# Kernel tuning notes

Hardware: AMD Instinct MI355X
Metric: run time of the kernel (lower is better)

## Reference

```python
import jax, jax.numpy as jnp
import numpy as np

B, T, NF, D = 512, 24, 81, 64
NH, HD = 4, 16
EPS = 1e-5


def _ln(x, g, b):
    m = x.mean(-1, keepdims=True)
    v = ((x - m) ** 2).mean(-1, keepdims=True)
    return (x - m) * jax.lax.rsqrt(v + EPS) * g + b


def _glu(h, w1, b1, w2, b2):
    return jax.nn.sigmoid(h @ w1 + b1) * (h @ w2 + b2)


def setup_inputs() -> dict:
    key = jax.random.key(0)
    ki = iter(jax.random.split(key, 64))

    def w(*shape):
        return jax.random.normal(next(ki), shape, jnp.float32) * 0.05

    FD = NF * D
    inp = {
        "x": jax.random.normal(next(ki), (B, T, NF), jnp.float32),
        # 81 per-feature GRNs, stacked along axis 0 (feature axis)
        "f_w1": w(NF, D), "f_b1": w(NF, D),
        "f_w2": w(NF, D, D), "f_b2": w(NF, D),
        "f_g1w": w(NF, D, D), "f_g1b": w(NF, D),
        "f_g2w": w(NF, D, D), "f_g2b": w(NF, D),
        "f_skw": w(NF, D), "f_skb": w(NF, D),
        "f_lng": jnp.ones((NF, D), jnp.float32), "f_lnb": jnp.zeros((NF, D), jnp.float32),
        # weight GRN: 5184 -> 64 -> 81
        "w_w1": w(FD, D), "w_b1": w(D),
        "w_w2": w(D, NF), "w_b2": w(NF),
        "w_g1w": w(NF, NF), "w_g1b": w(NF),
        "w_g2w": w(NF, NF), "w_g2b": w(NF),
        "w_skw": w(FD, NF), "w_skb": w(NF),
        "w_lng": jnp.ones((NF,), jnp.float32), "w_lnb": jnp.zeros((NF,), jnp.float32),
        # LSTM (torch layout: [4H, in], gate order i,f,g,o)
        "lstm_wih": w(4 * D, D), "lstm_whh": w(4 * D, D),
        "lstm_bih": w(4 * D), "lstm_bhh": w(4 * D),
        # post-lstm GLU + LN
        "pl_g1w": w(D, D), "pl_g1b": w(D), "pl_g2w": w(D, D), "pl_g2b": w(D),
        "pl_lng": jnp.ones((D,), jnp.float32), "pl_lnb": jnp.zeros((D,), jnp.float32),
        # MHA (in-proj packed q,k,v; weights stored [in, out])
        "attn_in_w": w(D, 3 * D), "attn_in_b": w(3 * D),
        "attn_out_w": w(D, D), "attn_out_b": w(D),
        # post-attn GLU + LN
        "pa_g1w": w(D, D), "pa_g1b": w(D), "pa_g2w": w(D, D), "pa_g2b": w(D),
        "pa_lng": jnp.ones((D,), jnp.float32), "pa_lnb": jnp.zeros((D,), jnp.float32),
        # feed-forward GRN (skip = identity since d_in == d_out)
        "ff_w1": w(D, 2 * D), "ff_b1": w(2 * D),
        "ff_w2": w(2 * D, D), "ff_b2": w(D),
        "ff_g1w": w(D, D), "ff_g1b": w(D), "ff_g2w": w(D, D), "ff_g2b": w(D),
        "ff_lng": jnp.ones((D,), jnp.float32), "ff_lnb": jnp.zeros((D,), jnp.float32),
        # output head
        "fc1_w": w(D, D), "fc1_b": w(D),
        "fc2_w": w(D, 6), "fc2_b": w(6),
    }
    return inp


def _forward(x, f_w1, f_b1, f_w2, f_b2, f_g1w, f_g1b, f_g2w, f_g2b, f_skw, f_skb,
             f_lng, f_lnb,
             w_w1, w_b1, w_w2, w_b2, w_g1w, w_g1b, w_g2w, w_g2b, w_skw, w_skb,
             w_lng, w_lnb,
             lstm_wih, lstm_whh, lstm_bih, lstm_bhh,
             pl_g1w, pl_g1b, pl_g2w, pl_g2b, pl_lng, pl_lnb,
             attn_in_w, attn_in_b, attn_out_w, attn_out_b,
             pa_g1w, pa_g1b, pa_g2w, pa_g2b, pa_lng, pa_lnb,
             ff_w1, ff_b1, ff_w2, ff_b2, ff_g1w, ff_g1b, ff_g2w, ff_g2b,
             ff_lng, ff_lnb,
             fc1_w, fc1_b, fc2_w, fc2_b):
    Bv, Tv = x.shape[0], x.shape[1]
    # --- VSN: 81 per-feature GRNs, vectorized over the feature axis ---
    h = jax.nn.elu(x[..., None] * f_w1 + f_b1)                    # [B,T,F,D]
    h = jnp.einsum('btfi,fio->btfo', h, f_w2) + f_b2
    h = jax.nn.sigmoid(jnp.einsum('btfi,fio->btfo', h, f_g1w) + f_g1b) \
        * (jnp.einsum('btfi,fio->btfo', h, f_g2w) + f_g2b)
    res = x[..., None] * f_skw + f_skb                            # skip: Linear(1,D)
    stacked = _ln(h + res, f_lng, f_lnb)                          # [B,T,F,D]
    flat = stacked.reshape(Bv, Tv, NF * D)
    # weight GRN -> softmax over features
    wh = jax.nn.elu(flat @ w_w1 + w_b1)
    wh = wh @ w_w2 + w_b2
    wh = _glu(wh, w_g1w, w_g1b, w_g2w, w_g2b)
    wnorm = _ln(wh + flat @ w_skw + w_skb, w_lng, w_lnb)
    weights = jax.nn.softmax(wnorm, axis=-1)                      # [B,T,F]
    selected = jnp.einsum('btfd,btf->btd', stacked, weights)      # [B,T,D]

    # --- LSTM encoder (single layer) ---
    def step(carry, xt):
        hp, cp = carry
        gates = xt @ lstm_wih.T + hp @ lstm_whh.T + lstm_bih + lstm_bhh
        i, f, g, o = jnp.split(gates, 4, axis=-1)
        c = jax.nn.sigmoid(f) * cp + jax.nn.sigmoid(i) * jnp.tanh(g)
        hn = jax.nn.sigmoid(o) * jnp.tanh(c)
        return (hn, c), hn

    h0 = jnp.zeros((Bv, D), x.dtype)
    _, hs = jax.lax.scan(step, (h0, h0), selected.transpose(1, 0, 2))
    lstm_out = hs.transpose(1, 0, 2)                              # [B,T,D]

    temporal = _ln(_glu(lstm_out, pl_g1w, pl_g1b, pl_g2w, pl_g2b) + selected,
                   pl_lng, pl_lnb)

    # --- Multi-head self-attention ---
    qkv = temporal @ attn_in_w + attn_in_b                        # [B,T,3D]
    q, k, v = jnp.split(qkv, 3, axis=-1)

    def heads(t):
        return t.reshape(Bv, Tv, NH, HD).transpose(0, 2, 1, 3)

    q, k, v = heads(q), heads(k), heads(v)
    scores = jnp.einsum('bhqd,bhkd->bhqk', q, k) / jnp.sqrt(jnp.float32(HD))
    a = jax.nn.softmax(scores, axis=-1)
    ao = jnp.einsum('bhqk,bhkd->bhqd', a, v).transpose(0, 2, 1, 3).reshape(Bv, Tv, D)
    attn_out = ao @ attn_out_w + attn_out_b

    enriched = _ln(_glu(attn_out, pa_g1w, pa_g1b, pa_g2w, pa_g2b) + temporal,
                   pa_lng, pa_lnb)

    # --- FF GRN (identity skip) ---
    fh = jax.nn.elu(enriched @ ff_w1 + ff_b1)
    fh = fh @ ff_w2 + ff_b2
    fh = _glu(fh, ff_g1w, ff_g1b, ff_g2w, ff_g2b)
    out = _ln(fh + enriched, ff_lng, ff_lnb)

    pooled = out.mean(axis=1)                                     # [B,D]
    return jax.nn.relu(pooled @ fc1_w + fc1_b) @ fc2_w + fc2_b    # [B,6]


def reference(x, f_w1, f_b1, f_w2, f_b2, f_g1w, f_g1b, f_g2w, f_g2b, f_skw, f_skb,
              f_lng, f_lnb,
              w_w1, w_b1, w_w2, w_b2, w_g1w, w_g1b, w_g2w, w_g2b, w_skw, w_skb,
              w_lng, w_lnb,
              lstm_wih, lstm_whh, lstm_bih, lstm_bhh,
              pl_g1w, pl_g1b, pl_g2w, pl_g2b, pl_lng, pl_lnb,
              attn_in_w, attn_in_b, attn_out_w, attn_out_b,
              pa_g1w, pa_g1b, pa_g2w, pa_g2b, pa_lng, pa_lnb,
              ff_w1, ff_b1, ff_w2, ff_b2, ff_g1w, ff_g1b, ff_g2w, ff_g2b,
              ff_lng, ff_lnb,
              fc1_w, fc1_b, fc2_w, fc2_b):
    return _forward(x, f_w1, f_b1, f_w2, f_b2, f_g1w, f_g1b, f_g2w, f_g2b, f_skw,
                    f_skb, f_lng, f_lnb, w_w1, w_b1, w_w2, w_b2, w_g1w, w_g1b,
                    w_g2w, w_g2b, w_skw, w_skb, w_lng, w_lnb, lstm_wih, lstm_whh,
                    lstm_bih, lstm_bhh, pl_g1w, pl_g1b, pl_g2w, pl_g2b, pl_lng,
                    pl_lnb, attn_in_w, attn_in_b, attn_out_w, attn_out_b, pa_g1w,
                    pa_g1b, pa_g2w, pa_g2b, pa_lng, pa_lnb, ff_w1, ff_b1, ff_w2,
                    ff_b2, ff_g1w, ff_g1b, ff_g2w, ff_g2b, ff_lng, ff_lnb, fc1_w,
                    fc1_b, fc2_w, fc2_b)
```

## Files before the change

### kernel.cpp

```cpp
#include <hip/hip_runtime.h>
#include <hip/hip_bf16.h>
#include <math.h>

constexpr int BB   = 512;
constexpr int TSEQ = 24;
constexpr int NF   = 81;
constexpr int DD   = 64;
constexpr int MTOT = BB * TSEQ;
constexpr int FDIM = NF * DD;
constexpr int KS   = 6;
constexpr int KSL  = 864;
constexpr int NW   = 160;
constexpr int NT   = 6;
constexpr float LN_EPS = 1e-5f;

typedef __attribute__((ext_vector_type(8))) short short8v;
typedef __attribute__((ext_vector_type(4))) float f32x4;

static __device__ __forceinline__ float sigmoidf_(float x) {
    return __builtin_amdgcn_rcpf(1.f + __expf(-x));
}
static __device__ __forceinline__ float eluf_(float x) {
    return x > 0.f ? x : (__expf(x) - 1.f);
}
static __device__ __forceinline__ float ftanh_(float x) {
    float e = __expf(2.f * x);
    return 1.f - 2.f * __builtin_amdgcn_rcpf(e + 1.f);
}
static __device__ __forceinline__ unsigned short f2bf(float x) {
    __hip_bfloat16 h = __float2bfloat16(x);
    return *reinterpret_cast<unsigned short*>(&h);
}
static __device__ __forceinline__ float b2f(unsigned short u) {
    __hip_bfloat16 h = *reinterpret_cast<__hip_bfloat16*>(&u);
    return __bfloat162float(h);
}

__global__ __launch_bounds__(256) void xt_kernel(
    const float* __restrict__ x, float* __restrict__ xT)
{
    __shared__ float tile[128 * 81];
    const int m0 = blockIdx.x * 128;
    const int t  = threadIdx.x;
    for (int e = t; e < 128 * 81; e += 256)
        tile[e] = x[(size_t)m0 * NF + e];
    __syncthreads();
    for (int e = t; e < 128 * 81; e += 256) {
        int f = e >> 7, r = e & 127;
        xT[(size_t)f * MTOT + m0 + r] = tile[r * 81 + f];
    }
}

__global__ __launch_bounds__(256) void vsn_kernel(
    const float* __restrict__ xT,
    const float* __restrict__ f_w1,  const float* __restrict__ f_b1,
    const float* __restrict__ f_w2,  const float* __restrict__ f_b2,
    const float* __restrict__ f_g1w, const float* __restrict__ f_g1b,
    const float* __restrict__ f_g2w, const float* __restrict__ f_g2b,
    const float* __restrict__ f_skw, const float* __restrict__ f_skb,
    const float* __restrict__ f_lng, const float* __restrict__ f_lnb,
    __hip_bfloat16* __restrict__ stacked)
{
    const int f  = blockIdx.y;
    const int t  = threadIdx.x;
    const int w  = t >> 6;
    const int l  = t & 63;
    const int lr = l & 15;
    const int lg = l >> 4;

    __shared__ __align__(16) unsigned short W2t[64 * 72];
    __shared__ __align__(16) unsigned short G1t[64 * 72];
    __shared__ __align__(16) unsigned short G2t[64 * 72];
    __shared__ __align__(16) unsigned short hS[4][16 * 72];
    __shared__ float vw1[64], vb1[64], vb2[64], vg1b[64], vg2b[64];
    __shared__ float vskw[64], vskb[64], vlng[64], vlnb[64];

    if (t < 64) {
        vw1[t]  = f_w1 [f*64 + t];  vb1[t]  = f_b1 [f*64 + t];
        vb2[t]  = f_b2 [f*64 + t];
        vg1b[t] = f_g1b[f*64 + t];  vg2b[t] = f_g2b[f*64 + t];
        vskw[t] = f_skw[f*64 + t];  vskb[t] = f_skb[f*64 + t];
        vlng[t] = f_lng[f*64 + t];  vlnb[t] = f_lnb[f*64 + t];
    }
    {
        const float* w2p = f_w2  + (size_t)f * 4096;
        const float* g1p = f_g1w + (size_t)f * 4096;
        const float* g2p = f_g2w + (size_t)f * 4096;
        #pragma unroll
        for (int p = 0; p < 16; ++p) {
            int e = t + 256 * p; int k = e >> 6, c = e & 63;
            W2t[c*72 + k] = f2bf(w2p[k*64 + c]);
            G1t[c*72 + k] = f2bf(g1p[k*64 + c]);
            G2t[c*72 + k] = f2bf(g2p[k*64 + c]);
        }
    }
    __syncthreads();

    unsigned short* slab = hS[w];

    for (int it = 0; it < NT; ++it) {
        const int m0 = (blockIdx.x * NT + it) * 64;
        const float xval = xT[(size_t)f * MTOT + m0 + w*16 + lr];

        short8v a0f, a1f;
        #pragma unroll
        for (int j = 0; j < 8; ++j) {
            const int d0 = lg*8 + j, d1 = 32 + lg*8 + j;
            a0f[j] = (short)f2bf(eluf_(xval * vw1[d0] + vb1[d0]));
            a1f[j] = (short)f2bf(eluf_(xval * vw1[d1] + vb1[d1]));
        }

        f32x4 acc1[4];
        #pragma unroll
        for (int cf = 0; cf < 4; ++cf) acc1[cf] = (f32x4){0.f,0.f,0.f,0.f};
        #pragma unroll
        for (int cf = 0; cf < 4; ++cf) {
            short8v b0 = *(const short8v*)&W2t[(cf*16 + lr)*72 + lg*8];
// ... 109 lines not shown
        short8v a0 = *(const short8v*)(stacked + a0r + k);
        short8v a1 = *(const short8v*)(stacked + a1r + k);
        #pragma unroll
        for (int n = 0; n < 10; ++n) {
            short8v bf = *(const short8v*)(WcatT + (size_t)(n*16 + lr) * FDIM + k);
            acc[0][n] = __builtin_amdgcn_mfma_f32_16x16x32_bf16(a0, bf, acc[0][n], 0, 0, 0);
            acc[1][n] = __builtin_amdgcn_mfma_f32_16x16x32_bf16(a1, bf, acc[1][n], 0, 0, 0);
        }
    }
    #pragma unroll
    for (int h = 0; h < 2; ++h)
        #pragma unroll
        for (int n = 0; n < 10; ++n)
            #pragma unroll
            for (int j = 0; j < 4; ++j) {
                const int m = m0 + h*16 + lg*4 + j;
                partial[((size_t)ks * mc + m) * NW + n*16 + lr] = acc[h][n][j];
            }
}

__global__ __launch_bounds__(256) void wtail_kernel(
    const float* __restrict__ partial,
    const __hip_bfloat16* __restrict__ stacked,
    const float* __restrict__ w_b1,  const float* __restrict__ w_skb,
    const float* __restrict__ w_w2,  const float* __restrict__ w_b2,
    const float* __restrict__ w_g1w, const float* __restrict__ w_g1b,
    const float* __restrict__ w_g2w, const float* __restrict__ w_g2b,
    const float* __restrict__ w_lng, const float* __restrict__ w_lnb,
    float* __restrict__ sel, __hip_bfloat16* __restrict__ selb, int mc)
{
    __shared__ float w2s[5184];
    __shared__ float g1s[6561];
    __shared__ float g2s[6561];
    __shared__ float sWh[16][64];
    __shared__ float sW2[16][96];
    __shared__ float wsh[16][81];

    const int t  = threadIdx.x;
    const int wv = t >> 6, l = t & 63;
    const int m0 = blockIdx.x * 16;
    const bool v1 = (l < 17);

    for (int e = t; e < 5184; e += 256) w2s[e] = w_w2[e];
    for (int e = t; e < 6561; e += 256) { g1s[e] = w_g1w[e]; g2s[e] = w_g2w[e]; }

    float s0[4], sk0[4], sk1[4];
    {
        const float b1v = w_b1[l], skb0 = w_skb[l], skb1 = v1 ? w_skb[64 + l] : 0.f;
        #pragma unroll
        for (int rr = 0; rr < 4; ++rr) { s0[rr] = b1v; sk0[rr] = skb0; sk1[rr] = skb1; }
    }
    #pragma unroll
    for (int ks = 0; ks < KS; ++ks) {
        #pragma unroll
        for (int rr = 0; rr < 4; ++rr) {
            const float* pr = partial + ((size_t)ks * mc + (m0 + wv*4 + rr)) * NW;
            s0[rr]  += pr[l];
            sk0[rr] += pr[64 + l];
            if (v1) sk1[rr] += pr[128 + l];
        }
    }
    #pragma unroll
    for (int rr = 0; rr < 4; ++rr) sWh[wv*4 + rr][l] = eluf_(s0[rr]);
    __syncthreads();

    float a0[4], a1[4];
    {
        const float b0 = w_b2[l], b1v = v1 ? w_b2[64 + l] : 0.f;
        #pragma unroll
        for (int rr = 0; rr < 4; ++rr) { a0[rr] = b0; a1[rr] = b1v; }
    }
    #pragma unroll 4
    for (int i = 0; i < 64; ++i) {
        const float wl = w2s[i*81 + l];
        const float wh = v1 ? w2s[i*81 + 64 + l] : 0.f;
        #pragma unroll
        for (int rr = 0; rr < 4; ++rr) {
            const float h = sWh[wv*4 + rr][i];
            a0[rr] += h * wl;
            a1[rr] += h * wh;
        }
    }
    #pragma unroll
    for (int rr = 0; rr < 4; ++rr) {
        sW2[wv*4 + rr][l] = a0[rr];
        if (v1) sW2[wv*4 + rr][64 + l] = a1[rr];
    }
    __syncthreads();

    float g10[4], g20[4], g11[4], g21[4];
    {
        const float c10 = w_g1b[l], c20 = w_g2b[l];
        const float c11 = v1 ? w_g1b[64 + l] : 0.f, c21 = v1 ? w_g2b[64 + l] : 0.f;
        #pragma unroll
        for (int rr = 0; rr < 4; ++rr) { g10[rr] = c10; g20[rr] = c20; g11[rr] = c11; g21[rr] = c21; }
    }
    #pragma unroll 3
    for (int i = 0; i < 81; ++i) {
        const float w1l = g1s[i*81 + l],            w2l = g2s[i*81 + l];
        const float w1h = v1 ? g1s[i*81 + 64 + l] : 0.f;
        const float w2h = v1 ? g2s[i*81 + 64 + l] : 0.f;
        #pragma unroll
        for (int rr = 0; rr < 4; ++rr) {
            const float h = sW2[wv*4 + rr][i];
            g10[rr] += h * w1l; g20[rr] += h * w2l;
            g11[rr] += h * w1h; g21[rr] += h * w2h;
        }
    }

    #pragma unroll
    for (int rr = 0; rr < 4; ++rr) {
        float y0 = sigmoidf_(g10[rr]) * g20[rr] + sk0[rr];
        float y1 = v1 ? (sigmoidf_(g11[rr]) * g21[rr] + sk1[rr]) : 0.f;

        float s = y0 + (v1 ? y1 : 0.f);
        #pragma unroll
        for (int off = 32; off; off >>= 1) s += __shfl_xor(s, off);
        const float mean = s / 81.f;
        float d0 = y0 - mean, d1 = v1 ? (y1 - mean) : 0.f;
        float vs = d0*d0 + (v1 ? d1*d1 : 0.f);
        #pragma unroll
        for (int off = 32; off; off >>= 1) vs += __shfl_xor(vs, off);
        const float inv = rsqrtf(vs / 81.f + LN_EPS);
        float wn0 = d0 * inv * w_lng[l] + w_lnb[l];
        float wn1 = v1 ? (d1 * inv * w_lng[64 + l] + w_lnb[64 + l]) : -1e30f;

        float mx = fmaxf(wn0, wn1);
        #pragma unroll
        for (int off = 32; off; off >>= 1) mx = fmaxf(mx, __shfl_xor(mx, off));
// ... 10 lines not shown
    {
        const int rr2 = t >> 4;
        const int d0 = (t & 15) * 4;
        const size_t mrow = (size_t)(m0 + rr2);
        float acc0 = 0.f, acc1f = 0.f, acc2 = 0.f, acc3 = 0.f;
        for (int f = 0; f < 81; ++f) {
            const float wv81 = wsh[rr2][f];
            ushort4 u = *(const ushort4*)&stacked[mrow * FDIM + f*64 + d0];
            acc0 += b2f(u.x) * wv81;
            acc1f += b2f(u.y) * wv81;
            acc2 += b2f(u.z) * wv81;
            acc3 += b2f(u.w) * wv81;
        }
        float4 ov = {acc0, acc1f, acc2, acc3};
        *(float4*)&sel[mrow * 64 + d0] = ov;
        ushort4 ub;
        ub.x = f2bf(acc0); ub.y = f2bf(acc1f); ub.z = f2bf(acc2); ub.w = f2bf(acc3);
        *(ushort4*)&((unsigned short*)selb)[mrow * 64 + d0] = ub;
    }
}

__global__ __launch_bounds__(256) void xw_kernel(
    const __hip_bfloat16* __restrict__ selb,
    const float* __restrict__ wih,
    const float* __restrict__ bih, const float* __restrict__ bhh,
    float* __restrict__ xW)
{
    const int m0 = blockIdx.x * 64;
    const int t = threadIdx.x;
    const int w = t >> 6, l = t & 63, lr = l & 15, lg = l >> 4;
    __shared__ __align__(16) unsigned short hA[64 * 72];
    __shared__ __align__(16) unsigned short Wt[256 * 72];
    __shared__ float vbs[256];

    vbs[t] = bih[t] + bhh[t];
    #pragma unroll
    for (int p = 0; p < 16; ++p) {
        int e = t + 256 * p; int r = e >> 6, d = e & 63;
        hA[r*72 + d] = *(const unsigned short*)&selb[(size_t)(m0 + r) * 64 + d];
    }
    #pragma unroll
    for (int p = 0; p < 64; ++p) {
        int e = t + 256 * p; int c = e >> 6, k = e & 63;
        Wt[c*72 + k] = f2bf(wih[c*64 + k]);
    }
    __syncthreads();

    f32x4 acc[4][4];
    #pragma unroll
    for (int rg = 0; rg < 4; ++rg)
        #pragma unroll
        for (int cf = 0; cf < 4; ++cf) acc[rg][cf] = (f32x4){0.f,0.f,0.f,0.f};
    #pragma unroll
    for (int ks = 0; ks < 2; ++ks) {
        short8v af[4];
        #pragma unroll
        for (int rg = 0; rg < 4; ++rg)
            af[rg] = *(const short8v*)&hA[(rg*16 + lr)*72 + ks*32 + lg*8];
        #pragma unroll
        for (int cf = 0; cf < 4; ++cf) {
            short8v bf = *(const short8v*)&Wt[(w*64 + cf*16 + lr)*72 + ks*32 + lg*8];
            #pragma unroll
            for (int rg = 0; rg < 4; ++rg)
                acc[rg][cf] = __builtin_amdgcn_mfma_f32_16x16x32_bf16(af[rg], bf, acc[rg][cf], 0, 0, 0);
        }
    }
    #pragma unroll
    for (int rg = 0; rg < 4; ++rg)
        #pragma unroll
        for (int cf = 0; cf < 4; ++cf)
            #pragma unroll
            for (int j = 0; j < 4; ++j) {
                int r = rg*16 + lg*4 + j, c = w*64 + cf*16 + lr;
                xW[(size_t)(m0 + r) * 256 + c] = acc[rg][cf][j] + vbs[c];
            }
}

__global__ __launch_bounds__(256) void batch_kernel(
    const float* __restrict__ xW, const float* __restrict__ whh,
    const float* __restrict__ sel,
    const float* __restrict__ pg1w, const float* __restrict__ pg1b,
    const float* __restrict__ pg2w, const float* __restrict__ pg2b,
    const float* __restrict__ plng, const float* __restrict__ plnb,
    const float* __restrict__ wqkv, const float* __restrict__ bqkv,
    const float* __restrict__ wout, const float* __restrict__ bout,
    const float* __restrict__ ag1w, const float* __restrict__ ag1b,
    const float* __restrict__ ag2w, const float* __restrict__ ag2b,
    const float* __restrict__ alng, const float* __restrict__ alnb,
    const float* __restrict__ fw1, const float* __restrict__ fb1,
    const float* __restrict__ fw2, const float* __restrict__ fb2,
    const float* __restrict__ fg1w, const float* __restrict__ fg1b,
    const float* __restrict__ fg2w, const float* __restrict__ fg2b,
    const float* __restrict__ flng, const float* __restrict__ flnb,
    const float* __restrict__ fc1_w, const float* __restrict__ fc1_b,
    const float* __restrict__ fc2_w, const float* __restrict__ fc2_b,
    float* __restrict__ out)
{
    const int b  = blockIdx.x;
    const int m0 = b * TSEQ;
    const int t  = threadIdx.x;
    const int w  = t >> 6, l = t & 63, lr = l & 15, lg = l >> 4;
    const int tr = t >> 4, tc = t & 15;

    __shared__ float tmpS[24 * 68];
    __shared__ float enrS[24 * 68];
    __shared__ __align__(16) unsigned short hA[32 * 72];
    __shared__ __align__(16) unsigned char U[27648];
    __shared__ float sh[64], sg[256];
    __shared__ float vpg1b[64], vpg2b[64], vplg[64], vplb[64];
    __shared__ float vob[64], vag1b[64], vag2b[64], valg[64], valb[64];
    __shared__ float vf1b[128], vf2b[64], vfg1b[64], vfg2b[64], vflg[64], vflb[64];

    unsigned short* Wt0 = (unsigned short*)U;
    unsigned short* Wt1 = (unsigned short*)(U + 9216);
    float*          yA  = (float*)(U + 18432);
// ... 22 lines not shown
    if (t < 64) sh[t] = 0.f;
    float c_reg = 0.f;
    float xnext = xW[(size_t)m0 * 256 + t];
    __syncthreads();

    for (int tt = 0; tt < TSEQ; ++tt) {
        float acc = xnext;
        if (tt + 1 < TSEQ)
            xnext = xW[(size_t)(m0 + tt + 1) * 256 + t];
        #pragma unroll
        for (int i = 0; i < 64; ++i) acc += sh[i] * wreg[i];
        sg[t] = acc;
        __syncthreads();
        if (t < 64) {
            float gi = sg[t], gf = sg[64 + t], gg = sg[128 + t], go = sg[192 + t];
            c_reg = sigmoidf_(gf) * c_reg + sigmoidf_(gi) * ftanh_(gg);
            float hn = sigmoidf_(go) * ftanh_(c_reg);
            sh[t] = hn;
            hA[tt*72 + t] = f2bf(hn);
        }
        __syncthreads();
    }

    #pragma unroll
    for (int p = 0; p < 16; ++p) {
        int e = t + 256 * p; int k = e >> 6, c = e & 63;
        Wt0[c*72 + k] = f2bf(pg1w[k*64 + c]);
        Wt1[c*72 + k] = f2bf(pg2w[k*64 + c]);
    }
    __syncthreads();

    f32x4 aA[2], aB[2];
    #pragma unroll
    for (int rg = 0; rg < 2; ++rg) { aA[rg] = (f32x4){0.f,0.f,0.f,0.f}; aB[rg] = (f32x4){0.f,0.f,0.f,0.f}; }
    #pragma unroll
    for (int ks = 0; ks < 2; ++ks) {
        short8v b0f = *(const short8v*)&Wt0[(w*16 + lr)*72 + ks*32 + lg*8];
        short8v b1f = *(const short8v*)&Wt1[(w*16 + lr)*72 + ks*32 + lg*8];
        #pragma unroll
        for (int rg = 0; rg < 2; ++rg) {
            short8v af = *(const short8v*)&hA[(rg*16 + lr)*72 + ks*32 + lg*8];
            aA[rg] = __builtin_amdgcn_mfma_f32_16x16x32_bf16(af, b0f, aA[rg], 0, 0, 0);
            aB[rg] = __builtin_amdgcn_mfma_f32_16x16x32_bf16(af, b1f, aB[rg], 0, 0, 0);
        }
    }
    float yv[2][4];
    #pragma unroll
    for (int rg = 0; rg < 2; ++rg)
        #pragma unroll
        for (int j = 0; j < 4; ++j) {
            int r = rg*16 + lg*4 + j, c = w*16 + lr;
// ... 18 lines not shown
        float4 v4 = *(const float4*)&yA[r*68 + tc*4];
        float part = v4.x + v4.y + v4.z + v4.w;
        #pragma unroll
        for (int off = 1; off < 16; off <<= 1) part += __shfl_xor(part, off);
        const float mean = part * (1.f / 64.f);
        float d0 = v4.x - mean, d1 = v4.y - mean, d2 = v4.z - mean, d3 = v4.w - mean;
        float vp = d0*d0 + d1*d1 + d2*d2 + d3*d3;
        #pragma unroll
        for (int off = 1; off < 16; off <<= 1) vp += __shfl_xor(vp, off);
        const float inv = rsqrtf(vp * (1.f / 64.f) + LN_EPS);
        const int c0 = tc * 4;
        float4 ov;
        ov.x = d0 * inv * vplg[c0+0] + vplb[c0+0];
        ov.y = d1 * inv * vplg[c0+1] + vplb[c0+1];
        ov.z = d2 * inv * vplg[c0+2] + vplb[c0+2];
        ov.w = d3 * inv * vplg[c0+3] + vplb[c0+3];
        if (r < TSEQ) *(float4*)&tmpS[r*68 + c0] = ov;
        ushort4 ob;
        ob.x = f2bf(ov.x); ob.y = f2bf(ov.y); ob.z = f2bf(ov.z); ob.w = f2bf(ov.w);
        *(ushort4*)&hA[r*72 + c0] = ob;
    }
    __syncthreads();

    #pragma unroll
    for (int p = 0; p < 48; ++p) {
        int e = t + 256 * p; int c = e >> 6, k = e & 63;
        Wq[c*72 + k] = f2bf(wqkv[(size_t)k * 192 + c]);
    }
    __syncthreads();

    f32x4 accq[2][3];
    #pragma unroll
    for (int rg = 0; rg < 2; ++rg)
        #pragma unroll
        for (int cf = 0; cf < 3; ++cf) accq[rg][cf] = (f32x4){0.f,0.f,0.f,0.f};
    #pragma unroll
    for (int ks = 0; ks < 2; ++ks) {
        short8v af[2];
        #pragma unroll
        for (int rg = 0; rg < 2; ++rg)
            af[rg] = *(const short8v*)&hA[(rg*16 + lr)*72 + ks*32 + lg*8];
        #pragma unroll
        for (int cf = 0; cf < 3; ++cf) {
            short8v bf = *(const short8v*)&Wq[(w*48 + cf*16 + lr)*72 + ks*32 + lg*8];
            #pragma unroll
            for (int rg = 0; rg < 2; ++rg)
                accq[rg][cf] = __builtin_amdgcn_mfma_f32_16x16x32_bf16(af[rg], bf, accq[rg][cf], 0, 0, 0);
        }
    }
    __syncthreads();
// ... 22 lines not shown
        for (int d = 0; d < 16; ++d) s += sq[(w*24 + i)*16 + d] * sk[(w*24 + j2)*16 + d];
        sp[(w*24 + i)*24 + j2] = s * 0.25f;
    }
    __syncthreads();
    if (l < 24) {
        float mx = -1e30f;
        for (int j = 0; j < 24; ++j) mx = fmaxf(mx, sp[(w*24 + l)*24 + j]);
        float s = 0.f;
        for (int j = 0; j < 24; ++j) { float e = __expf(sp[(w*24 + l)*24 + j] - mx); sp[(w*24 + l)*24 + j] = e; s += e; }
        float inv = __builtin_amdgcn_rcpf(s);
        for (int j = 0; j < 24; ++j) sp[(w*24 + l)*24 + j] *= inv;
    }
    __syncthreads();
    #pragma unroll
    for (int p = 0; p < 6; ++p) {
        int e = l + 64 * p; int ti = e >> 4, d = e & 15;
        float s = 0.f;
        #pragma unroll
        for (int j = 0; j < 24; ++j) s += sp[(w*24 + ti)*24 + j] * sv[(w*24 + j)*16 + d];
        hA[ti*72 + w*16 + d] = f2bf(s);
    }
    __syncthreads();

    #pragma unroll
    for (int p = 0; p < 16; ++p) {
        int e = t + 256 * p; int k = e >> 6, c = e & 63;
        Wt0[c*72 + k] = f2bf(wout[k*64 + c]);
    }
    __syncthreads();

    f32x4 acc1[2];
    #pragma unroll
    for (int rg = 0; rg < 2; ++rg) acc1[rg] = (f32x4){0.f,0.f,0.f,0.f};
    #pragma unroll
    for (int ks = 0; ks < 2; ++ks) {
        short8v bf = *(const short8v*)&Wt0[(w*16 + lr)*72 + ks*32 + lg*8];
        #pragma unroll
        for (int rg = 0; rg < 2; ++rg) {
            short8v af = *(const short8v*)&hA[(rg*16 + lr)*72 + ks*32 + lg*8];
            acc1[rg] = __builtin_amdgcn_mfma_f32_16x16x32_bf16(af, bf, acc1[rg], 0, 0, 0);
        }
    }
    #pragma unroll
    for (int p = 0; p < 16; ++p) {
        int e = t + 256 * p; int k = e >> 6, c = e & 63;
        Wt1[c*72 + k] = f2bf(ag1w[k*64 + c]);
    }
    __syncthreads();

    #pragma unroll
    for (int rg = 0; rg < 2; ++rg)
        #pragma unroll
        for (int j = 0; j < 4; ++j) {
            int r = rg*16 + lg*4 + j, c = w*16 + lr;
            hA[r*72 + c] = f2bf(acc1[rg][j] + vob[c]);
        }
    #pragma unroll
    for (int p = 0; p < 16; ++p) {
        int e = t + 256 * p; int k = e >> 6, c = e & 63;
        Wt0[c*72 + k] = f2bf(ag2w[k*64 + c]);
    }
    __syncthreads();

    #pragma unroll
    for (int rg = 0; rg < 2; ++rg) { aA[rg] = (f32x4){0.f,0.f,0.f,0.f}; aB[rg] = (f32x4){0.f,0.f,0.f,0.f}; }
    #pragma unroll
    for (int ks = 0; ks < 2; ++ks) {
        short8v b1f = *(const short8v*)&Wt1[(w*16 + lr)*72 + ks*32 + lg*8];
        short8v b2f = *(const short8v*)&Wt0[(w*16 + lr)*72 + ks*32 + lg*8];
        #pragma unroll
        for (int rg = 0; rg < 2; ++rg) {
            short8v af = *(const short8v*)&hA[(rg*16 + lr)*72 + ks*32 + lg*8];
            aA[rg] = __builtin_amdgcn_mfma_f32_16x16x32_bf16(af, b1f, aA[rg], 0, 0, 0);
            aB[rg] = __builtin_amdgcn_mfma_f32_16x16x32_bf16(af, b2f, aB[rg], 0, 0, 0);
        }
    }
    #pragma unroll
    for (int rg = 0; rg < 2; ++rg)
        #pragma unroll
        for (int j = 0; j < 4; ++j) {
            int r = rg*16 + lg*4 + j, c = w*16 + lr;
            int rc = r < TSEQ ? r : TSEQ - 1;
            float sgv = sigmoidf_(aA[rg][j] + vag1b[c]);
// ... 16 lines not shown
        float4 v4 = *(const float4*)&yA[r*68 + tc*4];
        float part = v4.x + v4.y + v4.z + v4.w;
        #pragma unroll
        for (int off = 1; off < 16; off <<= 1) part += __shfl_xor(part, off);
        const float mean = part * (1.f / 64.f);
        float d0 = v4.x - mean, d1 = v4.y - mean, d2 = v4.z - mean, d3 = v4.w - mean;
        float vp = d0*d0 + d1*d1 + d2*d2 + d3*d3;
        #pragma unroll
        for (int off = 1; off < 16; off <<= 1) vp += __shfl_xor(vp, off);
        const float inv = rsqrtf(vp * (1.f / 64.f) + LN_EPS);
        const int c0 = tc * 4;
        float4 ov;
        ov.x = d0 * inv * valg[c0+0] + valb[c0+0];
        ov.y = d1 * inv * valg[c0+1] + valb[c0+1];
        ov.z = d2 * inv * valg[c0+2] + valb[c0+2];
        ov.w = d3 * inv * valg[c0+3] + valb[c0+3];
        if (r < TSEQ) *(float4*)&enrS[r*68 + c0] = ov;
        ushort4 ob;
        ob.x = f2bf(ov.x); ob.y = f2bf(ov.y); ob.z = f2bf(ov.z); ob.w = f2bf(ov.w);
        *(ushort4*)&hA[r*72 + c0] = ob;
    }
    __syncthreads();

    #pragma unroll
    for (int p = 0; p < 32; ++p) {
        int e = t + 256 * p; int k = e >> 7, c = e & 127;
        W1t[c*72 + k] = f2bf(fw1[(size_t)k * 128 + c]);
    }
    __syncthreads();

    f32x4 accf[2][2];
    #pragma unroll
    for (int rg = 0; rg < 2; ++rg)
        #pragma unroll
        for (int cf = 0; cf < 2; ++cf) accf[rg][cf] = (f32x4){0.f,0.f,0.f,0.f};
    #pragma unroll
    for (int ks = 0; ks < 2; ++ks) {
        short8v af[2];
        #pragma unroll
        for (int rg = 0; rg < 2; ++rg)
            af[rg] = *(const short8v*)&hA[(rg*16 + lr)*72 + ks*32 + lg*8];
        #pragma unroll
        for (int cf = 0; cf < 2; ++cf) {
            short8v bf = *(const short8v*)&W1t[(w*32 + cf*16 + lr)*72 + ks*32 + lg*8];
            #pragma unroll
            for (int rg = 0; rg < 2; ++rg)
                accf[rg][cf] = __builtin_amdgcn_mfma_f32_16x16x32_bf16(af[rg], bf, accf[rg][cf], 0, 0, 0);
        }
    }
    __syncthreads();

    #pragma unroll
    for (int rg = 0; rg < 2; ++rg)
        #pragma unroll
        for (int cf = 0; cf < 2; ++cf)
            #pragma unroll
            for (int j = 0; j < 4; ++j) {
                int r = rg*16 + lg*4 + j, c = w*32 + cf*16 + lr;
                hBs[r*136 + c] = f2bf(eluf_(accf[rg][cf][j] + vf1b[c]));
            }
    #pragma unroll
    for (int p = 0; p < 32; ++p) {
        int e = t + 256 * p; int k = e >> 6, c = e & 63;
        W2t[c*136 + k] = f2bf(fw2[(size_t)k * 64 + c]);
    }
    __syncthreads();

    f32x4 acc2[2];
    #pragma unroll
    for (int rg = 0; rg < 2; ++rg) acc2[rg] = (f32x4){0.f,0.f,0.f,0.f};
    #pragma unroll
    for (int ks = 0; ks < 4; ++ks) {
        short8v bf = *(const short8v*)&W2t[(w*16 + lr)*136 + ks*32 + lg*8];
        #pragma unroll
        for (int rg = 0; rg < 2; ++rg) {
            short8v af = *(const short8v*)&hBs[(rg*16 + lr)*136 + ks*32 + lg*8];
            acc2[rg] = __builtin_amdgcn_mfma_f32_16x16x32_bf16(af, bf, acc2[rg], 0, 0, 0);
        }
    }
    #pragma unroll
    for (int rg = 0; rg < 2; ++rg)
        #pragma unroll
        for (int j = 0; j < 4; ++j) {
            int r = rg*16 + lg*4 + j, c = w*16 + lr;
            hA[r*72 + c] = f2bf(acc2[rg][j] + vf2b[c]);
        }
    __syncthreads();

    #pragma unroll
    for (int p = 0; p < 16; ++p) {
        int e = t + 256 * p; int k = e >> 6, c = e & 63;
        Wt0[c*72 + k] = f2bf(fg1w[k*64 + c]);
        Wt1[c*72 + k] = f2bf(fg2w[k*64 + c]);
    }
    __syncthreads();

    #pragma unroll
    for (int rg = 0; rg < 2; ++rg) { aA[rg] = (f32x4){0.f,0.f,0.f,0.f}; aB[rg] = (f32x4){0.f,0.f,0.f,0.f}; }
    #pragma unroll
    for (int ks = 0; ks < 2; ++ks) {
        short8v b1f = *(const short8v*)&Wt0[(w*16 + lr)*72 + ks*32 + lg*8];
        short8v b2f = *(const short8v*)&Wt1[(w*16 + lr)*72 + ks*32 + lg*8];
        #pragma unroll
        for (int rg = 0; rg < 2; ++rg) {
            short8v af = *(const short8v*)&hA[(rg*16 + lr)*72 + ks*32 + lg*8];
            aA[rg] = __builtin_amdgcn_mfma_f32_16x16x32_bf16(af, b1f, aA[rg], 0, 0, 0);
            aB[rg] = __builtin_amdgcn_mfma_f32_16x16x32_bf16(af, b2f, aB[rg], 0, 0, 0);
        }
    }
    #pragma unroll
    for (int rg = 0; rg < 2; ++rg)
        #pragma unroll
        for (int j = 0; j < 4; ++j) {
            int r = rg*16 + lg*4 + j, c = w*16 + lr;
            int rc = r < TSEQ ? r : TSEQ - 1;
            float sgv = sigmoidf_(aA[rg][j] + vfg1b[c]);
// ... 112 lines not shown
    const float* ff_g1w   = (const float*)d_in[49];
    const float* ff_g1b   = (const float*)d_in[50];
    const float* ff_g2w   = (const float*)d_in[51];
    const float* ff_g2b   = (const float*)d_in[52];
    const float* ff_lng   = (const float*)d_in[53];
    const float* ff_lnb   = (const float*)d_in[54];
    const float* fc1_w    = (const float*)d_in[55];
    const float* fc1_b    = (const float*)d_in[56];
    const float* fc2_w    = (const float*)d_in[57];
    const float* fc2_b    = (const float*)d_in[58];

    float* ws = (float*)d_ws;

    size_t o = 0;
    const size_t o_S0   = o; o += (size_t)MTOT * 256;
    o += (size_t)MTOT * 64;
    o += (size_t)MTOT * 64;
    o += (size_t)MTOT * 64;
    o += (size_t)MTOT * 64;
    o += (size_t)MTOT * 128;
    o += 16384;
    const size_t unionP2 = o;

    const size_t persist = (size_t)MTOT * 177;
    int mc = 0;
    {
        const int cands[4] = {12288, 6144, 3072, 1536};
        for (int ci = 0; ci < 4; ++ci) {
            const size_t c = (size_t)cands[ci];
            size_t overlay = c * FDIM / 2 + (size_t)KS * c * NW + c * 81
                           + (size_t)NW * FDIM / 2;
            size_t A = overlay > unionP2 ? overlay : unionP2;
            if ((A + persist) * sizeof(float) <= ws_size) { mc = cands[ci]; break; }
        }
        if (mc == 0) return;
    }
    const size_t ovl_partial = (size_t)mc * FDIM / 2;
    const size_t ovl_w81     = ovl_partial + (size_t)KS * mc * NW;
    const size_t ovl_wcat    = ovl_w81 + (size_t)mc * 81;
    const size_t ovl_end     = ovl_wcat + (size_t)NW * FDIM / 2;
    const size_t regA        = ovl_end > unionP2 ? ovl_end : unionP2;
    const size_t o_sel  = regA;
    const size_t o_selb = o_sel + (size_t)MTOT * 64;
    const size_t o_xt   = o_selb + (size_t)MTOT * 32;

    const dim3 blk(256);

    xt_kernel<<<dim3(MTOT / 128), blk, 0, stream>>>(x, ws + o_xt);
    wprep_kernel<<<dim3((FDIM + 255) / 256, NW), blk, 0, stream>>>(
        w_w1, w_skw, (unsigned short*)(ws + ovl_wcat));

    for (int mb = 0; mb < MTOT; mb += mc) {
        __hip_bfloat16* chunk = (__hip_bfloat16*)ws;
        vsn_kernel<<<dim3((mc / 64) / NT, NF), blk, 0, stream>>>(
            ws + o_xt + mb, f_w1, f_b1, f_w2, f_b2, f_g1w, f_g1b,
            f_g2w, f_g2b, f_skw, f_skb, f_lng, f_lnb, chunk);
        wgemm_kernel<<<dim3(mc / 32, KS), dim3(64), 0, stream>>>(
            chunk, (const unsigned short*)(ws + ovl_wcat), ws + ovl_partial, mc);
        wtail_kernel<<<dim3(mc / 16), blk, 0, stream>>>(
            ws + ovl_partial, chunk, w_b1, w_skb, w_w2, w_b2, w_g1w, w_g1b,
            w_g2w, w_g2b, w_lng, w_lnb,
            ws + o_sel + (size_t)mb * 64,
            (__hip_bfloat16*)(ws + o_selb) + (size_t)mb * 64, mc);
    }

    xw_kernel<<<dim3(MTOT / 64), blk, 0, stream>>>(
        (const __hip_bfloat16*)(ws + o_selb), lstm_wih, lstm_bih, lstm_bhh, ws + o_S0);
    batch_kernel<<<dim3(BB), blk, 0, stream>>>(
        ws + o_S0, lstm_whh, ws + o_sel,
        pl_g1w, pl_g1b, pl_g2w, pl_g2b, pl_lng, pl_lnb,
        attn_in_w, attn_in_b, attn_out_w, attn_out_b,
        pa_g1w, pa_g1b, pa_g2w, pa_g2b, pa_lng, pa_lnb,
        ff_w1, ff_b1, ff_w2, ff_b2, ff_g1w, ff_g1b, ff_g2w, ff_g2b,
        ff_lng, ff_lnb, fc1_w, fc1_b, fc2_w, fc2_b, (float*)d_out);
}
```

Before: 350.2 us.

## Pre-transpose and convert weights to bf16 once in a shared arena

Adds a one-time prep kernel that converts and transposes all per-feature GRN, LSTM input, and batch-kernel GLU/attention/FF weights into a bf16 arena in the workspace. Consumer kernels then copy pre-laid-out rows with 16-byte vector loads instead of each block doing strided fp32 loads, conversion and transposition. This removes redundant per-block conversion work, which is repeated across the 512 batch blocks and all VSN blocks. It costs one extra kernel launch plus arena space. The wtail weights are also stored in bf16, which halves their LDS footprint but lowers their precision.

After: 293.9 us. -16.1%, faster.

```diff
diff --git a/kernel.cpp b/kernel.cpp
--- a/kernel.cpp
+++ b/kernel.cpp
@@ -14,6 +14,23 @@
 constexpr int NT   = 6;
 constexpr float LN_EPS = 1e-5f;
 
+constexpr size_t AV    = 0;
+constexpr size_t AWIH  = 995328;
+constexpr size_t APL1  = 1011712;
+constexpr size_t APL2  = 1015808;
+constexpr size_t AWQ   = 1019904;
+constexpr size_t AWOUT = 1032192;
+constexpr size_t AAG1  = 1036288;
+constexpr size_t AAG2  = 1040384;
+constexpr size_t AFW1  = 1044480;
+constexpr size_t AFW2  = 1052672;
+constexpr size_t AFG1  = 1060864;
+constexpr size_t AFG2  = 1064960;
+constexpr size_t AW2S  = 1069056;
+constexpr size_t AG1S  = 1074240;
+constexpr size_t AG2S  = 1080801;
+constexpr size_t ATOT  = 1087362;
+
 typedef __attribute__((ext_vector_type(8))) short short8v;
 typedef __attribute__((ext_vector_type(4))) float f32x4;
 
@@ -51,12 +68,50 @@
     }
 }
 
+__global__ void wprep2_kernel(
+    const float* __restrict__ f_w2, const float* __restrict__ f_g1w,
+    const float* __restrict__ f_g2w, const float* __restrict__ wih,
+    const float* __restrict__ pg1w, const float* __restrict__ pg2w,
+    const float* __restrict__ wqkv, const float* __restrict__ wout,
+    const float* __restrict__ ag1w, const float* __restrict__ ag2w,
+    const float* __restrict__ fw1, const float* __restrict__ fw2,
+    const float* __restrict__ fg1w, const float* __restrict__ fg2w,
+    const float* __restrict__ w_w2, const float* __restrict__ w_g1w,
+    const float* __restrict__ w_g2w,
+    unsigned short* __restrict__ A)
+{
+    size_t i = (size_t)blockIdx.x * 256 + threadIdx.x;
+    if (i >= ATOT) return;
+    float v;
+    if (i < AWIH) {
+        size_t f = i / 12288; int r = (int)(i % 12288); int mat = r >> 12; int e = r & 4095;
+        int c = e >> 6, k = e & 63;
+        const float* src = mat == 0 ? f_w2 : (mat == 1 ? f_g1w : f_g2w);
+        v = src[f * 4096 + k * 64 + c];
+    }
+    else if (i < APL1) { v = wih[i - AWIH]; }
+    else if (i < APL2) { int e = (int)(i - APL1); int c = e >> 6, k = e & 63; v = pg1w[k*64 + c]; }
+    else if (i < AWQ)  { int e = (int)(i - APL2); int c = e >> 6, k = e & 63; v = pg2w[k*64 + c]; }
+    else if (i < AWOUT){ int e = (int)(i - AWQ);  int c = e >> 6, k = e & 63; v = wqkv[k*192 + c]; }
+    else if (i < AAG1) { int e = (int)(i - AWOUT);int c = e >> 6, k = e & 63; v = wout[k*64 + c]; }
+    else if (i < AAG2) { int e = (int)(i - AAG1); int c = e >> 6, k = e & 63; v = ag1w[k*64 + c]; }
+    else if (i < AFW1) { int e = (int)(i - AAG2); int c = e >> 6, k = e & 63; v = ag2w[k*64 + c]; }
+    else if (i < AFW2) { int e = (int)(i - AFW1); int c = e >> 6, k = e & 63; v = fw1[k*128 + c]; }
+    else if (i < AFG1) { int e = (int)(i - AFW2); int c = e >> 7, k = e & 127; v = fw2[k*64 + c]; }
+    else if (i < AFG2) { int e = (int)(i - AFG1); int c = e >> 6, k = e & 63; v = fg1w[k*64 + c]; }
+    else if (i < AW2S) { int e = (int)(i - AFG2); int c = e >> 6, k = e & 63; v = fg2w[k*64 + c]; }
+    else if (i < AG1S) { v = w_w2[i - AW2S]; }
+    else if (i < AG2S) { v = w_g1w[i - AG1S]; }
+    else               { v = w_g2w[i - AG2S]; }
+    A[i] = f2bf(v);
+}
+
 __global__ __launch_bounds__(256) void vsn_kernel(
     const float* __restrict__ xT,
+    const unsigned short* __restrict__ A,
     const float* __restrict__ f_w1,  const float* __restrict__ f_b1,
-    const float* __restrict__ f_w2,  const float* __restrict__ f_b2,
-    const float* __restrict__ f_g1w, const float* __restrict__ f_g1b,
-    const float* __restrict__ f_g2w, const float* __restrict__ f_g2b,
+    const float* __restrict__ f_b2,
+    const float* __restrict__ f_g1b, const float* __restrict__ f_g2b,
     const float* __restrict__ f_skw, const float* __restrict__ f_skb,
     const float* __restrict__ f_lng, const float* __restrict__ f_lnb,
     __hip_bfloat16* __restrict__ stacked)
@@ -83,16 +138,14 @@
         vlng[t] = f_lng[f*64 + t];  vlnb[t] = f_lnb[f*64 + t];
     }
     {
-        const float* w2p = f_w2  + (size_t)f * 4096;
-        const float* g1p = f_g1w + (size_t)f * 4096;
-        const float* g2p = f_g2w + (size_t)f * 4096;
-        #pragma unroll
-        for (int p = 0; p < 16; ++p) {
-            int e = t + 256 * p; int k = e >> 6, c = e & 63;
-            W2t[c*72 + k] = f2bf(w2p[k*64 + c]);
-            G1t[c*72 + k] = f2bf(g1p[k*64 + c]);
-            G2t[c*72 + k] = f2bf(g2p[k*64 + c]);
-        }
+        const unsigned short* av = A + (size_t)f * 12288;
+        const int c = t >> 2, k0 = (t & 3) * 16;
+        *(short8v*)&W2t[c*72 + k0]     = *(const short8v*)&av[c*64 + k0];
+        *(short8v*)&W2t[c*72 + k0 + 8] = *(const short8v*)&av[c*64 + k0 + 8];
+        *(short8v*)&G1t[c*72 + k0]     = *(const short8v*)&av[4096 + c*64 + k0];
+        *(short8v*)&G1t[c*72 + k0 + 8] = *(const short8v*)&av[4096 + c*64 + k0 + 8];
+        *(short8v*)&G2t[c*72 + k0]     = *(const short8v*)&av[8192 + c*64 + k0];
+        *(short8v*)&G2t[c*72 + k0 + 8] = *(const short8v*)&av[8192 + c*64 + k0 + 8];
     }
     __syncthreads();
 
@@ -248,16 +301,16 @@
 __global__ __launch_bounds__(256) void wtail_kernel(
     const float* __restrict__ partial,
     const __hip_bfloat16* __restrict__ stacked,
+    const unsigned short* __restrict__ A,
     const float* __restrict__ w_b1,  const float* __restrict__ w_skb,
-    const float* __restrict__ w_w2,  const float* __restrict__ w_b2,
-    const float* __restrict__ w_g1w, const float* __restrict__ w_g1b,
-    const float* __restrict__ w_g2w, const float* __restrict__ w_g2b,
+    const float* __restrict__ w_b2,
+    const float* __restrict__ w_g1b, const float* __restrict__ w_g2b,
     const float* __restrict__ w_lng, const float* __restrict__ w_lnb,
     float* __restrict__ sel, __hip_bfloat16* __restrict__ selb, int mc)
 {
-    __shared__ float w2s[5184];
-    __shared__ float g1s[6561];
-    __shared__ float g2s[6561];
+    __shared__ unsigned short w2h[5184];
+    __shared__ unsigned short g1h[6561];
+    __shared__ unsigned short g2h[6561];
     __shared__ float sWh[16][64];
     __shared__ float sW2[16][96];
     __shared__ float wsh[16][81];
@@ -267,8 +320,8 @@
     const int m0 = blockIdx.x * 16;
     const bool v1 = (l < 17);
 
-    for (int e = t; e < 5184; e += 256) w2s[e] = w_w2[e];
-    for (int e = t; e < 6561; e += 256) { g1s[e] = w_g1w[e]; g2s[e] = w_g2w[e]; }
+    for (int e = t; e < 5184; e += 256) w2h[e] = A[AW2S + e];
+    for (int e = t; e < 6561; e += 256) { g1h[e] = A[AG1S + e]; g2h[e] = A[AG2S + e]; }
 
     float s0[4], sk0[4], sk1[4];
     {
@@ -298,8 +351,8 @@
     }
     #pragma unroll 4
     for (int i = 0; i < 64; ++i) {
-        const float wl = w2s[i*81 + l];
-        const float wh = v1 ? w2s[i*81 + 64 + l] : 0.f;
+        const float wl = b2f(w2h[i*81 + l]);
+        const float wh = v1 ? b2f(w2h[i*81 + 64 + l]) : 0.f;
         #pragma unroll
         for (int rr = 0; rr < 4; ++rr) {
             const float h = sWh[wv*4 + rr][i];
@@ -323,14 +376,14 @@
     }
     #pragma unroll 3
     for (int i = 0; i < 81; ++i) {
-        const float w1l = g1s[i*81 + l],            w2l = g2s[i*81 + l];
-        const float w1h = v1 ? g1s[i*81 + 64 + l] : 0.f;
-        const float w2h = v1 ? g2s[i*81 + 64 + l] : 0.f;
+        const float w1l = b2f(g1h[i*81 + l]),        w2l = b2f(g2h[i*81 + l]);
+        const float w1h = v1 ? b2f(g1h[i*81 + 64 + l]) : 0.f;
+        const float w2h2 = v1 ? b2f(g2h[i*81 + 64 + l]) : 0.f;
         #pragma unroll
         for (int rr = 0; rr < 4; ++rr) {
             const float h = sW2[wv*4 + rr][i];
             g10[rr] += h * w1l; g20[rr] += h * w2l;
-            g11[rr] += h * w1h; g21[rr] += h * w2h;
+            g11[rr] += h * w1h; g21[rr] += h * w2h2;
         }
     }
 
@@ -387,7 +440,7 @@
 
 __global__ __launch_bounds__(256) void xw_kernel(
     const __hip_bfloat16* __restrict__ selb,
-    const float* __restrict__ wih,
+    const unsigned short* __restrict__ A,
     const float* __restrict__ bih, const float* __restrict__ bhh,
     float* __restrict__ xW)
 {
@@ -404,10 +457,11 @@
         int e = t + 256 * p; int r = e >> 6, d = e & 63;
         hA[r*72 + d] = *(const unsigned short*)&selb[(size_t)(m0 + r) * 64 + d];
     }
-    #pragma unroll
-    for (int p = 0; p < 64; ++p) {
-        int e = t + 256 * p; int c = e >> 6, k = e & 63;
-        Wt[c*72 + k] = f2bf(wih[c*64 + k]);
+    {
+        const int c = t;
+        #pragma unroll
+        for (int j = 0; j < 8; ++j)
+            *(short8v*)&Wt[c*72 + j*8] = *(const short8v*)&A[AWIH + (size_t)c*64 + j*8];
     }
     __syncthreads();
 
@@ -444,18 +498,14 @@
 __global__ __launch_bounds__(256) void batch_kernel(
     const float* __restrict__ xW, const float* __restrict__ whh,
     const float* __restrict__ sel,
-    const float* __restrict__ pg1w, const float* __restrict__ pg1b,
-    const float* __restrict__ pg2w, const float* __restrict__ pg2b,
+    const unsigned short* __restrict__ A,
+    const float* __restrict__ pg1b, const float* __restrict__ pg2b,
     const float* __restrict__ plng, const float* __restrict__ plnb,
-    const float* __restrict__ wqkv, const float* __restrict__ bqkv,
-    const float* __restrict__ wout, const float* __restrict__ bout,
-    const float* __restrict__ ag1w, const float* __restrict__ ag1b,
-    const float* __restrict__ ag2w, const float* __restrict__ ag2b,
+    const float* __restrict__ bqkv, const float* __restrict__ bout,
+    const float* __restrict__ ag1b, const float* __restrict__ ag2b,
     const float* __restrict__ alng, const float* __restrict__ alnb,
-    const float* __restrict__ fw1, const float* __restrict__ fb1,
-    const float* __restrict__ fw2, const float* __restrict__ fb2,
-    const float* __restrict__ fg1w, const float* __restrict__ fg1b,
-    const float* __restrict__ fg2w, const float* __restrict__ fg2b,
+    const float* __restrict__ fb1, const float* __restrict__ fb2,
+    const float* __restrict__ fg1b, const float* __restrict__ fg2b,
     const float* __restrict__ flng, const float* __restrict__ flnb,
     const float* __restrict__ fc1_w, const float* __restrict__ fc1_b,
     const float* __restrict__ fc2_w, const float* __restrict__ fc2_b,
@@ -524,11 +574,12 @@
         __syncthreads();
     }
 
-    #pragma unroll
-    for (int p = 0; p < 16; ++p) {
-        int e = t + 256 * p; int k = e >> 6, c = e & 63;
-        Wt0[c*72 + k] = f2bf(pg1w[k*64 + c]);
-        Wt1[c*72 + k] = f2bf(pg2w[k*64 + c]);
+    {
+        const int c = t >> 2, k0 = (t & 3) * 16;
+        *(short8v*)&Wt0[c*72+k0]   = *(const short8v*)&A[APL1 + c*64 + k0];
+        *(short8v*)&Wt0[c*72+k0+8] = *(const short8v*)&A[APL1 + c*64 + k0 + 8];
+        *(short8v*)&Wt1[c*72+k0]   = *(const short8v*)&A[APL2 + c*64 + k0];
+        *(short8v*)&Wt1[c*72+k0+8] = *(const short8v*)&A[APL2 + c*64 + k0 + 8];
     }
     __syncthreads();
 
@@ -593,10 +644,10 @@
     }
     __syncthreads();
 
-    #pragma unroll
-    for (int p = 0; p < 48; ++p) {
-        int e = t + 256 * p; int c = e >> 6, k = e & 63;
-        Wq[c*72 + k] = f2bf(wqkv[(size_t)k * 192 + c]);
+    if (t < 192) {
+        #pragma unroll
+        for (int j = 0; j < 8; ++j)
+            *(short8v*)&Wq[t*72 + j*8] = *(const short8v*)&A[AWQ + (size_t)t*64 + j*8];
     }
     __syncthreads();
 
@@ -665,10 +716,10 @@
     }
     __syncthreads();
 
-    #pragma unroll
-    for (int p = 0; p < 16; ++p) {
-        int e = t + 256 * p; int k = e >> 6, c = e & 63;
-        Wt0[c*72 + k] = f2bf(wout[k*64 + c]);
+    {
+        const int c = t >> 2, k0 = (t & 3) * 16;
+        *(short8v*)&Wt0[c*72+k0]   = *(const short8v*)&A[AWOUT + c*64 + k0];
+        *(short8v*)&Wt0[c*72+k0+8] = *(const short8v*)&A[AWOUT + c*64 + k0 + 8];
     }
     __syncthreads();
 
@@ -684,10 +735,10 @@
             acc1[rg] = __builtin_amdgcn_mfma_f32_16x16x32_bf16(af, bf, acc1[rg], 0, 0, 0);
         }
     }
-    #pragma unroll
-    for (int p = 0; p < 16; ++p) {
-        int e = t + 256 * p; int k = e >> 6, c = e & 63;
-        Wt1[c*72 + k] = f2bf(ag1w[k*64 + c]);
+    {
+        const int c = t >> 2, k0 = (t & 3) * 16;
+        *(short8v*)&Wt1[c*72+k0]   = *(const short8v*)&A[AAG1 + c*64 + k0];
+        *(short8v*)&Wt1[c*72+k0+8] = *(const short8v*)&A[AAG1 + c*64 + k0 + 8];
     }
     __syncthreads();
 
@@ -698,10 +749,10 @@
             int r = rg*16 + lg*4 + j, c = w*16 + lr;
             hA[r*72 + c] = f2bf(acc1[rg][j] + vob[c]);
         }
-    #pragma unroll
-    for (int p = 0; p < 16; ++p) {
-        int e = t + 256 * p; int k = e >> 6, c = e & 63;
-        Wt0[c*72 + k] = f2bf(ag2w[k*64 + c]);
+    {
+        const int c = t >> 2, k0 = (t & 3) * 16;
+        *(short8v*)&Wt0[c*72+k0]   = *(const short8v*)&A[AAG2 + c*64 + k0];
+        *(short8v*)&Wt0[c*72+k0+8] = *(const short8v*)&A[AAG2 + c*64 + k0 + 8];
     }
     __syncthreads();
 
@@ -764,10 +815,11 @@
     }
     __syncthreads();
 
-    #pragma unroll
-    for (int p = 0; p < 32; ++p) {
-        int e = t + 256 * p; int k = e >> 7, c = e & 127;
-        W1t[c*72 + k] = f2bf(fw1[(size_t)k * 128 + c]);
+    {
+        const int c = t >> 1, k0 = (t & 1) * 32;
+        #pragma unroll
+        for (int j = 0; j < 4; ++j)
+            *(short8v*)&W1t[c*72 + k0 + j*8] = *(const short8v*)&A[AFW1 + (size_t)c*64 + k0 + j*8];
     }
     __syncthreads();
 
@@ -801,10 +853,11 @@
                 int r = rg*16 + lg*4 + j, c = w*32 + cf*16 + lr;
                 hBs[r*136 + c] = f2bf(eluf_(accf[rg][cf][j] + vf1b[c]));
             }
-    #pragma unroll
-    for (int p = 0; p < 32; ++p) {
-        int e = t + 256 * p; int k = e >> 6, c = e & 63;
-        W2t[c*136 + k] = f2bf(fw2[(size_t)k * 64 + c]);
+    {
+        const int c = t >> 2, k0 = (t & 3) * 32;
+        #pragma unroll
+        for (int j = 0; j < 4; ++j)
+            *(short8v*)&W2t[c*136 + k0 + j*8] = *(const short8v*)&A[AFW2 + (size_t)c*128 + k0 + j*8];
     }
     __syncthreads();
 
@@ -829,11 +882,12 @@
         }
     __syncthreads();
 
-    #pragma unroll
-    for (int p = 0; p < 16; ++p) {
-        int e = t + 256 * p; int k = e >> 6, c = e & 63;
-        Wt0[c*72 + k] = f2bf(fg1w[k*64 + c]);
-        Wt1[c*72 + k] = f2bf(fg2w[k*64 + c]);
+    {
+        const int c = t >> 2, k0 = (t & 3) * 16;
+        *(short8v*)&Wt0[c*72+k0]   = *(const short8v*)&A[AFG1 + c*64 + k0];
+        *(short8v*)&Wt0[c*72+k0+8] = *(const short8v*)&A[AFG1 + c*64 + k0 + 8];
+        *(short8v*)&Wt1[c*72+k0]   = *(const short8v*)&A[AFG2 + c*64 + k0];
+        *(short8v*)&Wt1[c*72+k0+8] = *(const short8v*)&A[AFG2 + c*64 + k0 + 8];
     }
     __syncthreads();
 
@@ -992,7 +1046,8 @@
     o += 16384;
     const size_t unionP2 = o;
 
-    const size_t persist = (size_t)MTOT * 177;
+    const size_t arenaF = (ATOT + 2) / 2 + 64;
+    const size_t persist = (size_t)MTOT * 177 + arenaF;
     int mc = 0;
     {
         const int cands[4] = {12288, 6144, 3072, 1536};
@@ -1000,8 +1055,8 @@
             const size_t c = (size_t)cands[ci];
             size_t overlay = c * FDIM / 2 + (size_t)KS * c * NW + c * 81
                            + (size_t)NW * FDIM / 2;
-            size_t A = overlay > unionP2 ? overlay : unionP2;
-            if ((A + persist) * sizeof(float) <= ws_size) { mc = cands[ci]; break; }
+            size_t A0 = overlay > unionP2 ? overlay : unionP2;
+            if ((A0 + persist) * sizeof(float) <= ws_size) { mc = cands[ci]; break; }
         }
         if (mc == 0) return;
     }
@@ -1010,37 +1065,41 @@
     const size_t ovl_wcat    = ovl_w81 + (size_t)mc * 81;
     const size_t ovl_end     = ovl_wcat + (size_t)NW * FDIM / 2;
     const size_t regA        = ovl_end > unionP2 ? ovl_end : unionP2;
-    const size_t o_sel  = regA;
-    const size_t o_selb = o_sel + (size_t)MTOT * 64;
-    const size_t o_xt   = o_selb + (size_t)MTOT * 32;
+    const size_t o_sel   = regA;
+    const size_t o_selb  = o_sel + (size_t)MTOT * 64;
+    const size_t o_xt    = o_selb + (size_t)MTOT * 32;
+    const size_t o_arena = o_xt + (size_t)NF * MTOT;
+    unsigned short* Ar = (unsigned short*)(ws + o_arena);
 
     const dim3 blk(256);
 
     xt_kernel<<<dim3(MTOT / 128), blk, 0, stream>>>(x, ws + o_xt);
     wprep_kernel<<<dim3((FDIM + 255) / 256, NW), blk, 0, stream>>>(
         w_w1, w_skw, (unsigned short*)(ws + ovl_wcat));
+    wprep2_kernel<<<dim3((int)((ATOT + 255) / 256)), blk, 0, stream>>>(
+        f_w2, f_g1w, f_g2w, lstm_wih, pl_g1w, pl_g2w, attn_in_w, attn_out_w,
+        pa_g1w, pa_g2w, ff_w1, ff_w2, ff_g1w, ff_g2w, w_w2, w_g1w, w_g2w, Ar);
 
     for (int mb = 0; mb < MTOT; mb += mc) {
         __hip_bfloat16* chunk = (__hip_bfloat16*)ws;
         vsn_kernel<<<dim3((mc / 64) / NT, NF), blk, 0, stream>>>(
-            ws + o_xt + mb, f_w1, f_b1, f_w2, f_b2, f_g1w, f_g1b,
-            f_g2w, f_g2b, f_skw, f_skb, f_lng, f_lnb, chunk);
+            ws + o_xt + mb, Ar, f_w1, f_b1, f_b2, f_g1b, f_g2b,
+            f_skw, f_skb, f_lng, f_lnb, chunk);
         wgemm_kernel<<<dim3(mc / 32, KS), dim3(64), 0, stream>>>(
             chunk, (const unsigned short*)(ws + ovl_wcat), ws + ovl_partial, mc);
         wtail_kernel<<<dim3(mc / 16), blk, 0, stream>>>(
-            ws + ovl_partial, chunk, w_b1, w_skb, w_w2, w_b2, w_g1w, w_g1b,
-            w_g2w, w_g2b, w_lng, w_lnb,
+            ws + ovl_partial, chunk, Ar, w_b1, w_skb, w_b2, w_g1b, w_g2b,
+            w_lng, w_lnb,
             ws + o_sel + (size_t)mb * 64,
             (__hip_bfloat16*)(ws + o_selb) + (size_t)mb * 64, mc);
     }
 
     xw_kernel<<<dim3(MTOT / 64), blk, 0, stream>>>(
-        (const __hip_bfloat16*)(ws + o_selb), lstm_wih, lstm_bih, lstm_bhh, ws + o_S0);
+        (const __hip_bfloat16*)(ws + o_selb), Ar, lstm_bih, lstm_bhh, ws + o_S0);
     batch_kernel<<<dim3(BB), blk, 0, stream>>>(
-        ws + o_S0, lstm_whh, ws + o_sel,
-        pl_g1w, pl_g1b, pl_g2w, pl_g2b, pl_lng, pl_lnb,
-        attn_in_w, attn_in_b, attn_out_w, attn_out_b,
-        pa_g1w, pa_g1b, pa_g2w, pa_g2b, pa_lng, pa_lnb,
-        ff_w1, ff_b1, ff_w2, ff_b2, ff_g1w, ff_g1b, ff_g2w, ff_g2b,
-        ff_lng, ff_lnb, fc1_w, fc1_b, fc2_w, fc2_b, (float*)d_out);
-}
+        ws + o_S0, lstm_whh, ws + o_sel, Ar,
+        pl_g1b, pl_g2b, pl_lng, pl_lnb,
+        attn_in_b, attn_out_b, pa_g1b, pa_g2b, pa_lng, pa_lnb,
+        ff_b1, ff_b2, ff_g1b, ff_g2b, ff_lng, ff_lnb,
+        fc1_w, fc1_b, fc2_w, fc2_b, (float*)d_out);
+}
```
